# Kernel optimization log

Measured on AMD Instinct MI355X. Metric: run time of the kernel, lower is better.

Reference implementation:

```python
import jax, jax.numpy as jnp
import numpy as np

N, E, EQ = 100000, 600000, 200000
F_IN, HID, N_CONVS = 128, 128, 4  # n_layers=3 -> 4 conv blocks
BN_EPS = 1e-5


def setup_inputs() -> dict:
    key = jax.random.key(0)
    ks = jax.random.split(key, 16)
    s = 1.0 / np.sqrt(HID)
    inp = {
        "x": jax.random.normal(ks[0], (N, F_IN), jnp.float32),
        "edge_index": jax.random.randint(ks[1], (2, E), 0, N, jnp.int64),
        "edge_attr": jax.random.uniform(ks[2], (E,), jnp.float32),
        "edge_label_index": jax.random.randint(ks[3], (2, EQ), 0, N, jnp.int64),
        # GraphConv params (layer 0 has in_dim == hidden_dim, so stack all 4)
        "rel_w": jax.random.normal(ks[4], (N_CONVS, HID, HID), jnp.float32) * s,
        "rel_b": jnp.zeros((N_CONVS, HID), jnp.float32),
        "root_w": jax.random.normal(ks[5], (N_CONVS, HID, HID), jnp.float32) * s,
        "bn_g": jnp.ones((N_CONVS, HID), jnp.float32),
        "bn_b": jnp.zeros((N_CONVS, HID), jnp.float32),
        # edge MLP: Linear(2H->H), GELU, Linear(H->1)
        "mlp_w1": jax.random.normal(ks[6], (2 * HID, HID), jnp.float32) * (1.0 / np.sqrt(2 * HID)),
        "mlp_b1": jnp.zeros((HID,), jnp.float32),
        "mlp_w2": jax.random.normal(ks[7], (HID, 1), jnp.float32) * s,
        "mlp_b2": jnp.zeros((1,), jnp.float32),
    }
    return inp


def reference(x, edge_index, edge_attr, edge_label_index,
              rel_w, rel_b, root_w, bn_g, bn_b,
              mlp_w1, mlp_b1, mlp_w2, mlp_b2):
    src, dst = edge_index[0], edge_index[1]
    n = x.shape[0]
    for l in range(rel_w.shape[0]):
        # GraphConv: lin_rel(sum_j w_ij * x_j) + lin_root(x_i)
        msg = x[src] * edge_attr[:, None]                      # [E, H] gather
        agg = jax.ops.segment_sum(msg, dst, num_segments=n)    # [N, H] scatter-add
        h = agg @ rel_w[l] + rel_b[l] + x @ root_w[l]
        h = jax.nn.gelu(h, approximate=False)
        # BatchNorm over nodes (training-mode batch stats, biased var)
        mean = h.mean(axis=0)
        var = h.var(axis=0)
        x = (h - mean) * jax.lax.rsqrt(var + BN_EPS) * bn_g[l] + bn_b[l]
    ef = jnp.concatenate([x[edge_label_index[0]], x[edge_label_index[1]]], axis=-1)  # [EQ, 2H]
    hmid = jax.nn.gelu(ef @ mlp_w1 + mlp_b1, approximate=False)
    out = jax.nn.sigmoid(hmid @ mlp_w2 + mlp_b2)
    return out.squeeze(-1)
```

## Files before the change

### kernel.cpp

```cpp
#include <hip/hip_runtime.h>

#define NN 100000
#define EE 600000
#define NQ 200000
#define HID 128
#define NL 4
#define BN_EPS 1e-5f
#define ECAP 1280

typedef __attribute__((ext_vector_type(8))) short short8;
typedef __attribute__((ext_vector_type(4))) float f32x4;

__device__ __forceinline__ float gelu_f(float v) {
    return 0.5f * v * (1.0f + erff(v * 0.70710678118654752f));
}
__device__ __forceinline__ unsigned short f2bf(float f) {
    unsigned int x = __float_as_uint(f);
    unsigned int r = (x + 0x7FFFu + ((x >> 16) & 1u)) >> 16;
    return (unsigned short)r;
}
__device__ __forceinline__ float bf2f(unsigned short u) {
    return __uint_as_float(((unsigned int)u) << 16);
}


__global__ void k_zero_int(int* __restrict__ p, int n) {
    int i = blockIdx.x * blockDim.x + threadIdx.x;
    if (i < n) p[i] = 0;
}

__global__ void k_cvt(const float* __restrict__ x, unsigned int* __restrict__ o, int n2) {
    int i = blockIdx.x * blockDim.x + threadIdx.x;
    if (i < n2) {
        float2 v = ((const float2*)x)[i];
        o[i] = (unsigned int)f2bf(v.x) | ((unsigned int)f2bf(v.y) << 16);
    }
}

__global__ void k_bninit(float* __restrict__ sc) {
    int i = threadIdx.x;
    sc[i] = (i < 128) ? 1.0f : 0.0f;
}


__global__ void k_hist(const int* __restrict__ ei, int* __restrict__ cnt) {
    int e = blockIdx.x * blockDim.x + threadIdx.x;
    if (e < EE) atomicAdd(&cnt[ei[EE + e]], 1);
}

__global__ void k_scan1(const int* __restrict__ cnt, int* __restrict__ rp,
                        int* __restrict__ bsum, int n) {
    __shared__ int sh[256];
    const int tid = threadIdx.x;
    const int base = blockIdx.x * 1024;
    int v[4];
    int s = 0;
    #pragma unroll
    for (int j = 0; j < 4; ++j) {
        int idx = base + tid * 4 + j;
        v[j] = (idx < n) ? cnt[idx] : 0;
        s += v[j];
    }
    sh[tid] = s;
    __syncthreads();
    for (int off = 1; off < 256; off <<= 1) {
        int t = (tid >= off) ? sh[tid - off] : 0;
        __syncthreads();
        sh[tid] += t;
        __syncthreads();
    }
    int run = sh[tid] - s;
    #pragma unroll
    for (int j = 0; j < 4; ++j) {
        int idx = base + tid * 4 + j;
        if (idx < n) rp[idx] = run;
        run += v[j];
    }
    if (tid == 255) bsum[blockIdx.x] = sh[255];
}

__global__ void k_scan2(int* __restrict__ bsum, int nb) {
    __shared__ int sh[256];
    const int tid = threadIdx.x;
    int v = (tid < nb) ? bsum[tid] : 0;
    sh[tid] = v;
    __syncthreads();
    for (int off = 1; off < 256; off <<= 1) {
        int t = (tid >= off) ? sh[tid - off] : 0;
        __syncthreads();
        sh[tid] += t;
        __syncthreads();
    }
    if (tid < nb) bsum[tid] = sh[tid] - v;
}

__global__ void k_scan3(int* __restrict__ rp, const int* __restrict__ bsum,
                        int* __restrict__ cnt, int n) {
    int i = blockIdx.x * blockDim.x + threadIdx.x;
    if (i < n) {
        rp[i] += bsum[i >> 10];
        cnt[i] = 0;
    }
    if (i == 0) rp[n] = EE;
}

__global__ void k_fill(const int* __restrict__ ei, const int* __restrict__ rp,
                       int* __restrict__ cur, int* __restrict__ eord) {
    int e = blockIdx.x * blockDim.x + threadIdx.x;
    if (e < EE) {
        int d = ei[EE + e];
        int p = rp[d] + atomicAdd(&cur[d], 1);
        eord[p] = e;
    }
}

__global__ void k_sortfill(const int* __restrict__ ei, const float* __restrict__ ea,
                           const int* __restrict__ rp, int* __restrict__ eord,
                           int* __restrict__ csrc, float* __restrict__ cea,
                           float* __restrict__ wdeg) {
    int n = blockIdx.x * blockDim.x + threadIdx.x;
    if (n >= NN) return;
    const int s0 = rp[n], s1 = rp[n + 1];
    for (int i = s0 + 1; i < s1; ++i) {
        int key = eord[i];
        int j = i - 1;
        while (j >= s0 && eord[j] > key) { eord[j + 1] = eord[j]; --j; }
        eord[j + 1] = key;
    }
    float s = 0.f;
    for (int i = s0; i < s1; ++i) {
        const int e = eord[i];
        csrc[i] = ei[e];
        const float w = ea[e];
        cea[i] = w;
        s += w;
    }
    wdeg[n] = s;
}


__global__ void k_wprep(const float* __restrict__ relw, const float* __restrict__ rootw,
                        const float* __restrict__ relb, const float* __restrict__ sc,
                        unsigned short* __restrict__ Wtf, float* __restrict__ bias2,
                        float* __restrict__ brel) {
    __shared__ float shb[256];
    const int n = blockIdx.x;
    const int k = threadIdx.x;
    const float s = sc[k & 127];
    const float w = (k < 128) ? relw[(size_t)k * HID + n] : rootw[(size_t)(k - 128) * HID + n];
    const int nb = n >> 4, l15 = n & 15;
    const int kc = k >> 5, kg = (k >> 3) & 3, e = k & 7;
    Wtf[((size_t)(kc * 8 + nb) * 512) + (kg * 16 + l15) * 8 + e] = f2bf(s * w);
    shb[k] = sc[128 + (k & 127)] * w;
    __syncthreads();
    #pragma unroll
    for (int off = 64; off >= 1; off >>= 1) {
        if (k < off) shb[k] += shb[k + off];
        else if (k >= 128 && k < 128 + off) shb[k] += shb[k + off];
        __syncthreads();
    }
    if (k == 0) brel[n] = shb[0];
    if (k == 128) bias2[n] = relb[n] + shb[128];
}

__global__ void k_mlpprep(const float* __restrict__ w1, const float* __restrict__ b1,
                          const float* __restrict__ sc, unsigned short* __restrict__ Wtmf,
                          float* __restrict__ b1v) {
    __shared__ float shb[256];
    const int n = blockIdx.x;
    const int k = threadIdx.x;
    const float w = w1[(size_t)k * HID + n];
    const int nb = n >> 4, l15 = n & 15;
    const int kc = k >> 5, kg = (k >> 3) & 3, e = k & 7;
    Wtmf[((size_t)(kc * 8 + nb) * 512) + (kg * 16 + l15) * 8 + e] = f2bf(sc[k & 127] * w);
    shb[k] = sc[128 + (k & 127)] * w;
    __syncthreads();
    #pragma unroll
    for (int off = 128; off >= 1; off >>= 1) {
        if (k < off) shb[k] += shb[k + off];
        __syncthreads();
    }
    if (k == 0) b1v[n] = b1[n] + shb[0];
}


__global__ __launch_bounds__(512, 6) void k_gemm2(
    const unsigned short* __restrict__ hprev, const int* __restrict__ csrc,
    const float* __restrict__ cea, const int* __restrict__ rp,
    const unsigned short* __restrict__ Wtf, const float* __restrict__ bias2,
    const float* __restrict__ brel, const float* __restrict__ wdeg,
    unsigned short* __restrict__ hnext, float* __restrict__ bnpart,
    int nrows, int nblk) {
    __shared__ unsigned short As[128 * 128];
    __shared__ float psb[8 * 64];
    __shared__ float pqb[8 * 64];
    __shared__ int eidx[ECAP];
    __shared__ float ew[ECAP];
    __shared__ int rps[132];
    const int tid = threadIdx.x;
    const int rb = blockIdx.x * 128;

    const int lane = tid & 63;
    const int wid = tid >> 6;
    const int wm = wid >> 1, wn = wid & 1;

    if (tid < 129) {
        int nn = rb + tid;
        rps[tid] = rp[nn < nrows ? nn : nrows];
    }
    __syncthreads();
    const int e0 = rps[0];
    const int ne = rps[128] - e0;
    const bool useLds = (ne <= ECAP);
    if (useLds) {
        for (int i = tid; i < ne; i += 512) {
            eidx[i] = csrc[e0 + i];
            ew[i] = cea[e0 + i];
        }
    }

    f32x4 acc[2][4];
    #pragma unroll
    for (int mf = 0; mf < 2; ++mf)
        #pragma unroll
        for (int nf = 0; nf < 4; ++nf) acc[mf][nf] = (f32x4){0.f, 0.f, 0.f, 0.f};

    #pragma unroll
    for (int s = 0; s < 2; ++s) {
        __syncthreads();
        if (s == 0) {
            const int g = lane >> 4;
            const int cl = lane & 15;
            for (int rr = 0; rr < 16; ++rr) {
                const int r = wid * 16 + rr;
                const int s0 = rps[r] - e0, s1 = rps[r + 1] - e0;
                float a0 = 0.f, a1 = 0.f, a2 = 0.f, a3 = 0.f,
                      a4 = 0.f, a5 = 0.f, a6 = 0.f, a7 = 0.f;
                for (int i = s0 + g; i < s1; i += 8) {
                    const int i2 = i + 4;
                    const bool has2 = i2 < s1;
                    int src1, src2;
                    float w1, w2;
                    if (useLds) {
                        src1 = eidx[i]; w1 = ew[i];
                        src2 = has2 ? eidx[i2] : src1;
                        w2 = has2 ? ew[i2] : 0.f;
                    } else {
                        src1 = csrc[e0 + i]; w1 = cea[e0 + i];
                        src2 = has2 ? csrc[e0 + i2] : src1;
                        w2 = has2 ? cea[e0 + i2] : 0.f;
                    }
                    const uint4 va = *(const uint4*)(hprev + (size_t)src1 * HID + cl * 8);
                    const uint4 vb = *(const uint4*)(hprev + (size_t)src2 * HID + cl * 8);
                    a0 += bf2f((unsigned short)(va.x)) * w1;
                    a1 += bf2f((unsigned short)(va.x >> 16)) * w1;
                    a2 += bf2f((unsigned short)(va.y)) * w1;
                    a3 += bf2f((unsigned short)(va.y >> 16)) * w1;
                    a4 += bf2f((unsigned short)(va.z)) * w1;
                    a5 += bf2f((unsigned short)(va.z >> 16)) * w1;
                    a6 += bf2f((unsigned short)(va.w)) * w1;
                    a7 += bf2f((unsigned short)(va.w >> 16)) * w1;
                    a0 += bf2f((unsigned short)(vb.x)) * w2;
                    a1 += bf2f((unsigned short)(vb.x >> 16)) * w2;
                    a2 += bf2f((unsigned short)(vb.y)) * w2;
                    a3 += bf2f((unsigned short)(vb.y >> 16)) * w2;
                    a4 += bf2f((unsigned short)(vb.z)) * w2;
                    a5 += bf2f((unsigned short)(vb.z >> 16)) * w2;
                    a6 += bf2f((unsigned short)(vb.w)) * w2;
                    a7 += bf2f((unsigned short)(vb.w >> 16)) * w2;
                }
                a0 += __shfl_xor(a0, 16); a1 += __shfl_xor(a1, 16);
                a2 += __shfl_xor(a2, 16); a3 += __shfl_xor(a3, 16);
                a4 += __shfl_xor(a4, 16); a5 += __shfl_xor(a5, 16);
                a6 += __shfl_xor(a6, 16); a7 += __shfl_xor(a7, 16);
                a0 += __shfl_xor(a0, 32); a1 += __shfl_xor(a1, 32);
                a2 += __shfl_xor(a2, 32); a3 += __shfl_xor(a3, 32);
                a4 += __shfl_xor(a4, 32); a5 += __shfl_xor(a5, 32);
                a6 += __shfl_xor(a6, 32); a7 += __shfl_xor(a7, 32);
                if (g == 0) {
                    uint4 o;
                    o.x = (unsigned int)f2bf(a0) | ((unsigned int)f2bf(a1) << 16);
                    o.y = (unsigned int)f2bf(a2) | ((unsigned int)f2bf(a3) << 16);
                    o.z = (unsigned int)f2bf(a4) | ((unsigned int)f2bf(a5) << 16);
                    o.w = (unsigned int)f2bf(a6) | ((unsigned int)f2bf(a7) << 16);
                    const int p = cl ^ (r & 7);
                    *(uint4*)(As + r * 128 + p * 8) = o;
                }
            }
        } else {
            #pragma unroll
            for (int i = 0; i < 4; ++i) {
                const int r = i * 32 + (tid >> 4);
                const int p = tid & 15;
                const int gr = min(rb + r, nrows - 1);
                const int gc = p ^ (r & 7);
                const uint4 v = *(const uint4*)(hprev + (size_t)gr * 128 + gc * 8);
                *(uint4*)(As + r * 128 + p * 8) = v;
            }
        }
        __syncthreads();
        #pragma unroll
        for (int kk = 0; kk < 4; ++kk) {
            short8 a[2], b[4];
            #pragma unroll
            for (int mf = 0; mf < 2; ++mf) {
                const int r = wm * 32 + mf * 16 + (lane & 15);
                const int p = (kk * 4 + (lane >> 4)) ^ (r & 7);
                a[mf] = *(const short8*)(As + r * 128 + p * 8);
            }
            #pragma unroll
            for (int nf = 0; nf < 4; ++nf) {
                b[nf] = *(const short8*)(Wtf + ((size_t)((s * 4 + kk) * 8 + wn * 4 + nf) * 512)
                                               + lane * 8);
            }
            #pragma unroll
            for (int mf = 0; mf < 2; ++mf)
                #pragma unroll
                for (int nf = 0; nf < 4; ++nf)
                    acc[mf][nf] = __builtin_amdgcn_mfma_f32_16x16x32_bf16(
                        a[mf], b[nf], acc[mf][nf], 0, 0, 0);
        }
    }

    __syncthreads();

    int colv[4];
    float biasv[4], brelv[4];
    #pragma unroll
    for (int nf = 0; nf < 4; ++nf) {
        colv[nf] = wn * 64 + nf * 16 + (lane & 15);
        biasv[nf] = bias2[colv[nf]];
        brelv[nf] = brel[colv[nf]];
    }
    float ps[4] = {0.f, 0.f, 0.f, 0.f}, pq[4] = {0.f, 0.f, 0.f, 0.f};
    #pragma unroll
    for (int mf = 0; mf < 2; ++mf) {
        #pragma unroll
        for (int reg = 0; reg < 4; ++reg) {
            const int lr = wm * 32 + mf * 16 + (lane >> 4) * 4 + reg;
            const int gm = rb + lr;
            const bool valid = gm < nrows;
            const float wd = valid ? wdeg[gm] : 0.f;
            #pragma unroll
            for (int nf = 0; nf < 4; ++nf) {
                const float hv = gelu_f(acc[mf][nf][reg] + biasv[nf] + wd * brelv[nf]);
                As[lr * 128 + colv[nf]] = f2bf(hv);
                if (valid) {
                    ps[nf] += hv;
                    pq[nf] += hv * hv;
                }
            }
        }
    }
    #pragma unroll
    for (int nf = 0; nf < 4; ++nf) {
        ps[nf] += __shfl_xor(ps[nf], 16); ps[nf] += __shfl_xor(ps[nf], 32);
        pq[nf] += __shfl_xor(pq[nf], 16); pq[nf] += __shfl_xor(pq[nf], 32);
        if ((lane >> 4) == 0) {
            psb[wid * 64 + nf * 16 + (lane & 15)] = ps[nf];
            pqb[wid * 64 + nf * 16 + (lane & 15)] = pq[nf];
        }
    }
    __syncthreads();

    const int nvalid = nrows - rb;
    #pragma unroll
    for (int it = 0; it < 4; ++it) {
        const int r = it * 32 + (tid >> 4);
        const int c16 = tid & 15;
        if (r < nvalid)
            *(uint4*)(hnext + (size_t)(rb + r) * 128 + c16 * 8) =
                *(const uint4*)(As + r * 128 + c16 * 8);
    }
    if (tid < 128) {
        const int wnh = tid >> 6;
        const int c64 = tid & 63;
        float s = 0.f, q = 0.f;
        #pragma unroll
        for (int w = 0; w < 4; ++w) {
            s += psb[(w * 2 + wnh) * 64 + c64];
            q += pqb[(w * 2 + wnh) * 64 + c64];
        }
        bnpart[(size_t)tid * nblk + blockIdx.x] = s;
        bnpart[(size_t)(128 + tid) * nblk + blockIdx.x] = q;
    }
}

__global__ void k_bnredfin(const float* __restrict__ bnpart, int nblk,
                           const float* __restrict__ g, const float* __restrict__ b,
                           float* __restrict__ sc) {
    __shared__ float sh[256];
    __shared__ float sh2[256];
    const int tid = threadIdx.x;
    const int col = blockIdx.x;
    float s = 0.f, q = 0.f;
    for (int i = tid; i < nblk; i += 256) {
        s += bnpart[(size_t)col * nblk + i];
        q += bnpart[(size_t)(128 + col) * nblk + i];
    }
    sh[tid] = s;
    sh2[tid] = q;
    __syncthreads();
    #pragma unroll
    for (int off = 128; off >= 1; off >>= 1) {
        if (tid < off) { sh[tid] += sh[tid + off]; sh2[tid] += sh2[tid + off]; }
        __syncthreads();
    }
    if (tid == 0) {
        const float inv_n = 1.0f / (float)NN;
        const float mean = sh[0] * inv_n;
        const float var = sh2[0] * inv_n - mean * mean;
        const float scale = g[col] * rsqrtf(var + BN_EPS);
        sc[col] = scale;
        sc[128 + col] = b[col] - mean * scale;
    }
}


__global__ __launch_bounds__(512, 6) void k_mlp2(
    const unsigned short* __restrict__ xf, const int* __restrict__ eli,
    const unsigned short* __restrict__ Wtmf, const float* __restrict__ b1v,
    const float* __restrict__ w2, const float* __restrict__ b2,
    float* __restrict__ out, int nq) {
    __shared__ unsigned short As[128 * 128];
    __shared__ int sidx[256];
    __shared__ float rowred2[2][128];
    const int tid = threadIdx.x;
    const int qb = blockIdx.x * 128;
    if (tid < 256) {
        const int rr = tid & 127;
        const int q = qb + rr;
        sidx[tid] = (q < nq) ? eli[(tid >> 7) * NQ + q] : 0;
    }
    __syncthreads();

    const int lane = tid & 63;
    const int wid = tid >> 6;
    const int wm = wid >> 1, wn = wid & 1;

    f32x4 acc[2][4];
    #pragma unroll
    for (int mf = 0; mf < 2; ++mf)
        #pragma unroll
        for (int nf = 0; nf < 4; ++nf) acc[mf][nf] = (f32x4){0.f, 0.f, 0.f, 0.f};

    #pragma unroll
    for (int s = 0; s < 2; ++s) {
        if (s) __syncthreads();
        #pragma unroll
        for (int i = 0; i < 4; ++i) {
            const int r = i * 32 + (tid >> 4);
            const int p = tid & 15;
            const int node = sidx[s * 128 + r];
            const int gc = p ^ (r & 7);
            const uint4 v = *(const uint4*)(xf + (size_t)node * 128 + gc * 8);
            *(uint4*)(As + r * 128 + p * 8) = v;
        }
        __syncthreads();
        #pragma unroll
        for (int kk = 0; kk < 4; ++kk) {
            short8 a[2], b[4];
            #pragma unroll
            for (int mf = 0; mf < 2; ++mf) {
                const int r = wm * 32 + mf * 16 + (lane & 15);
                const int p = (kk * 4 + (lane >> 4)) ^ (r & 7);
                a[mf] = *(const short8*)(As + r * 128 + p * 8);
            }
            #pragma unroll
            for (int nf = 0; nf < 4; ++nf) {
                b[nf] = *(const short8*)(Wtmf + ((size_t)((s * 4 + kk) * 8 + wn * 4 + nf) * 512)
                                               + lane * 8);
            }
            #pragma unroll
            for (int mf = 0; mf < 2; ++mf)
                #pragma unroll
                for (int nf = 0; nf < 4; ++nf)
                    acc[mf][nf] = __builtin_amdgcn_mfma_f32_16x16x32_bf16(
                        a[mf], b[nf], acc[mf][nf], 0, 0, 0);
        }
    }

    int colv[4];
    float w2v[4], b1c[4];
    #pragma unroll
    for (int nf = 0; nf < 4; ++nf) {
        colv[nf] = wn * 64 + nf * 16 + (lane & 15);
        w2v[nf] = w2[colv[nf]];
        b1c[nf] = b1v[colv[nf]];
    }
    #pragma unroll
    for (int mf = 0; mf < 2; ++mf) {
        #pragma unroll
        for (int reg = 0; reg < 4; ++reg) {
            float part = 0.f;
            #pragma unroll
            for (int nf = 0; nf < 4; ++nf)
                part += gelu_f(acc[mf][nf][reg] + b1c[nf]) * w2v[nf];
            part += __shfl_xor(part, 1);
            part += __shfl_xor(part, 2);
            part += __shfl_xor(part, 4);
            part += __shfl_xor(part, 8);
            if ((lane & 15) == 0) {
                const int lr = wm * 32 + mf * 16 + (lane >> 4) * 4 + reg;
                rowred2[wn][lr] = part;
            }
        }
    }
    __syncthreads();
    if (tid < 128) {
        const int q = qb + tid;
        if (q < nq)
            out[q] = 1.0f / (1.0f + expf(-(rowred2[0][tid] + rowred2[1][tid] + b2[0])));
    }
}


extern "C" void kernel_launch(void* const* d_in, const int* in_sizes, int n_in,
                              void* d_out, int out_size, void* d_ws, size_t ws_size,
                              hipStream_t stream) {
    const float* x_in = (const float*)d_in[0];
    const int* ei = (const int*)d_in[1];
    const float* ea = (const float*)d_in[2];
    const int* eli = (const int*)d_in[3];
    const float* rel_w = (const float*)d_in[4];
    const float* rel_b = (const float*)d_in[5];
    const float* root_w = (const float*)d_in[6];
    const float* bn_g = (const float*)d_in[7];
    const float* bn_b = (const float*)d_in[8];
    const float* w1 = (const float*)d_in[9];
    const float* b1 = (const float*)d_in[10];
    const float* w2 = (const float*)d_in[11];
    const float* b2 = (const float*)d_in[12];
    float* out = (float*)d_out;

    char* ws = (char*)d_ws;
    size_t off = 0;
    auto alloc = [&](size_t bytes) -> void* {
        void* p = ws + off;
        off = (off + bytes + 255) & ~(size_t)255;
        return p;
    };
    const int nblk_gemm = (NN + 127) / 128;
    unsigned short* hb0 = (unsigned short*)alloc(2ull * NN * HID);
    unsigned short* hb1 = (unsigned short*)alloc(2ull * NN * HID);
    int* eord = (int*)alloc(sizeof(int) * EE);
    int* csrc = (int*)alloc(sizeof(int) * EE);
    float* cea = (float*)alloc(sizeof(float) * EE);
    int* rp = (int*)alloc(sizeof(int) * (NN + 1));
    int* cnt = (int*)alloc(sizeof(int) * NN);
    int* bsum = (int*)alloc(sizeof(int) * 256);
    float* wdeg = (float*)alloc(sizeof(float) * NN);
    float* bnpart = (float*)alloc(sizeof(float) * 256 * (size_t)nblk_gemm);
    float* bnsc = (float*)alloc(sizeof(float) * 256);
    unsigned short* Wtf = (unsigned short*)alloc(2ull * 128 * 256);
    unsigned short* Wtmf = (unsigned short*)alloc(2ull * 128 * 256);
    float* bias2 = (float*)alloc(sizeof(float) * 128);
    float* brel = (float*)alloc(sizeof(float) * 128);
    float* b1v = (float*)alloc(sizeof(float) * 128);
    (void)ws_size;

    const int nb_scan = (NN + 1023) / 1024;

    k_cvt<<<(NN * 64 + 255) / 256, 256, 0, stream>>>(x_in, (unsigned int*)hb0, NN * 64);

    k_zero_int<<<(NN + 255) / 256, 256, 0, stream>>>(cnt, NN);
    k_hist<<<(EE + 255) / 256, 256, 0, stream>>>(ei, cnt);
    k_scan1<<<nb_scan, 256, 0, stream>>>(cnt, rp, bsum, NN);
    k_scan2<<<1, 256, 0, stream>>>(bsum, nb_scan);
    k_scan3<<<(NN + 255) / 256, 256, 0, stream>>>(rp, bsum, cnt, NN);
    k_fill<<<(EE + 255) / 256, 256, 0, stream>>>(ei, rp, cnt, eord);
    k_sortfill<<<(NN + 255) / 256, 256, 0, stream>>>(ei, ea, rp, eord, csrc, cea, wdeg);
    k_bninit<<<1, 256, 0, stream>>>(bnsc);

    unsigned short* hcur = hb0;
    unsigned short* bufs[2] = {hb1, hb0};
    for (int l = 0; l < NL; ++l) {
        unsigned short* hnext = bufs[l & 1];
        k_wprep<<<128, 256, 0, stream>>>(rel_w + (size_t)l * HID * HID,
                                         root_w + (size_t)l * HID * HID,
                                         rel_b + (size_t)l * HID, bnsc, Wtf, bias2, brel);
        k_gemm2<<<nblk_gemm, 512, 0, stream>>>(hcur, csrc, cea, rp, Wtf, bias2, brel, wdeg,
                                               hnext, bnpart, NN, nblk_gemm);
        k_bnredfin<<<128, 256, 0, stream>>>(bnpart, nblk_gemm,
                                            bn_g + (size_t)l * HID, bn_b + (size_t)l * HID, bnsc);
        hcur = hnext;
    }

    k_mlpprep<<<128, 256, 0, stream>>>(w1, b1, bnsc, Wtmf, b1v);
    k_mlp2<<<(NQ + 127) / 128, 512, 0, stream>>>(hcur, eli, Wtmf, b1v, w2, b2, out, NQ);
}
```

Baseline: 461.1 us.

## Assign one row per 16-lane group in gather, pack edge data, store output directly

The aggregation phase now gives each 16-lane quarter-wave its own destination row instead of splitting each row's edges across four lane groups. This removes the cross-group shuffle reductions and the lane-0-only write, and uses two independent accumulator sets to keep dependent adds apart. Edge source index and weight are packed into one int2 LDS array so a single LDS load fetches both. The epilogue writes bf16 results straight to global memory as scattered 2-byte stores instead of staging through LDS for coalesced 16-byte writes, which lets one barrier go. The risk is load imbalance between rows of different degree within a wave, and poorer coalescing of the output stores.

```diff
diff --git a/kernel.cpp b/kernel.cpp
--- a/kernel.cpp
+++ b/kernel.cpp
@@ -194,8 +194,7 @@
     __shared__ unsigned short As[128 * 128];
     __shared__ float psb[8 * 64];
     __shared__ float pqb[8 * 64];
-    __shared__ int eidx[ECAP];
-    __shared__ float ew[ECAP];
+    __shared__ int2 ewi[ECAP];
     __shared__ int rps[132];
     const int tid = threadIdx.x;
     const int rb = blockIdx.x * 128;
@@ -214,8 +213,7 @@
     const bool useLds = (ne <= ECAP);
     if (useLds) {
         for (int i = tid; i < ne; i += 512) {
-            eidx[i] = csrc[e0 + i];
-            ew[i] = cea[e0 + i];
+            ewi[i] = make_int2(csrc[e0 + i], __float_as_int(cea[e0 + i]));
         }
     }
 
@@ -231,24 +229,27 @@
         if (s == 0) {
             const int g = lane >> 4;
             const int cl = lane & 15;
-            for (int rr = 0; rr < 16; ++rr) {
-                const int r = wid * 16 + rr;
+            #pragma unroll
+            for (int rs = 0; rs < 4; ++rs) {
+                const int r = wid * 16 + rs * 4 + g;
                 const int s0 = rps[r] - e0, s1 = rps[r + 1] - e0;
                 float a0 = 0.f, a1 = 0.f, a2 = 0.f, a3 = 0.f,
                       a4 = 0.f, a5 = 0.f, a6 = 0.f, a7 = 0.f;
-                for (int i = s0 + g; i < s1; i += 8) {
-                    const int i2 = i + 4;
-                    const bool has2 = i2 < s1;
+                float c0 = 0.f, c1 = 0.f, c2 = 0.f, c3 = 0.f,
+                      c4 = 0.f, c5 = 0.f, c6 = 0.f, c7 = 0.f;
+                for (int i = s0; i < s1; i += 2) {
                     int src1, src2;
                     float w1, w2;
+                    const bool has2 = (i + 1) < s1;
                     if (useLds) {
-                        src1 = eidx[i]; w1 = ew[i];
-                        src2 = has2 ? eidx[i2] : src1;
-                        w2 = has2 ? ew[i2] : 0.f;
+                        const int2 p1 = ewi[i];
+                        src1 = p1.x; w1 = __int_as_float(p1.y);
+                        const int2 p2 = has2 ? ewi[i + 1] : p1;
+                        src2 = p2.x; w2 = has2 ? __int_as_float(p2.y) : 0.f;
                     } else {
                         src1 = csrc[e0 + i]; w1 = cea[e0 + i];
-                        src2 = has2 ? csrc[e0 + i2] : src1;
-                        w2 = has2 ? cea[e0 + i2] : 0.f;
+                        src2 = has2 ? csrc[e0 + i + 1] : src1;
+                        w2 = has2 ? cea[e0 + i + 1] : 0.f;
                     }
                     const uint4 va = *(const uint4*)(hprev + (size_t)src1 * HID + cl * 8);
                     const uint4 vb = *(const uint4*)(hprev + (size_t)src2 * HID + cl * 8);
@@ -260,32 +261,24 @@
                     a5 += bf2f((unsigned short)(va.z >> 16)) * w1;
                     a6 += bf2f((unsigned short)(va.w)) * w1;
                     a7 += bf2f((unsigned short)(va.w >> 16)) * w1;
-                    a0 += bf2f((unsigned short)(vb.x)) * w2;
-                    a1 += bf2f((unsigned short)(vb.x >> 16)) * w2;
-                    a2 += bf2f((unsigned short)(vb.y)) * w2;
-                    a3 += bf2f((unsigned short)(vb.y >> 16)) * w2;
-                    a4 += bf2f((unsigned short)(vb.z)) * w2;
-                    a5 += bf2f((unsigned short)(vb.z >> 16)) * w2;
-                    a6 += bf2f((unsigned short)(vb.w)) * w2;
-                    a7 += bf2f((unsigned short)(vb.w >> 16)) * w2;
+                    c0 += bf2f((unsigned short)(vb.x)) * w2;
+                    c1 += bf2f((unsigned short)(vb.x >> 16)) * w2;
+                    c2 += bf2f((unsigned short)(vb.y)) * w2;
+                    c3 += bf2f((unsigned short)(vb.y >> 16)) * w2;
+                    c4 += bf2f((unsigned short)(vb.z)) * w2;
+                    c5 += bf2f((unsigned short)(vb.z >> 16)) * w2;
+                    c6 += bf2f((unsigned short)(vb.w)) * w2;
+                    c7 += bf2f((unsigned short)(vb.w >> 16)) * w2;
                 }
-                a0 += __shfl_xor(a0, 16); a1 += __shfl_xor(a1, 16);
-                a2 += __shfl_xor(a2, 16); a3 += __shfl_xor(a3, 16);
-                a4 += __shfl_xor(a4, 16); a5 += __shfl_xor(a5, 16);
-                a6 += __shfl_xor(a6, 16); a7 += __shfl_xor(a7, 16);
-                a0 += __shfl_xor(a0, 32); a1 += __shfl_xor(a1, 32);
-                a2 += __shfl_xor(a2, 32); a3 += __shfl_xor(a3, 32);
-                a4 += __shfl_xor(a4, 32); a5 += __shfl_xor(a5, 32);
-                a6 += __shfl_xor(a6, 32); a7 += __shfl_xor(a7, 32);
-                if (g == 0) {
-                    uint4 o;
-                    o.x = (unsigned int)f2bf(a0) | ((unsigned int)f2bf(a1) << 16);
-                    o.y = (unsigned int)f2bf(a2) | ((unsigned int)f2bf(a3) << 16);
-                    o.z = (unsigned int)f2bf(a4) | ((unsigned int)f2bf(a5) << 16);
-                    o.w = (unsigned int)f2bf(a6) | ((unsigned int)f2bf(a7) << 16);
-                    const int p = cl ^ (r & 7);
-                    *(uint4*)(As + r * 128 + p * 8) = o;
-                }
+                a0 += c0; a1 += c1; a2 += c2; a3 += c3;
+                a4 += c4; a5 += c5; a6 += c6; a7 += c7;
+                uint4 o;
+                o.x = (unsigned int)f2bf(a0) | ((unsigned int)f2bf(a1) << 16);
+                o.y = (unsigned int)f2bf(a2) | ((unsigned int)f2bf(a3) << 16);
+                o.z = (unsigned int)f2bf(a4) | ((unsigned int)f2bf(a5) << 16);
+                o.w = (unsigned int)f2bf(a6) | ((unsigned int)f2bf(a7) << 16);
+                const int p = cl ^ (r & 7);
+                *(uint4*)(As + r * 128 + p * 8) = o;
             }
         } else {
             #pragma unroll
@@ -322,8 +315,6 @@
         }
     }
 
-    __syncthreads();
-
     int colv[4];
     float biasv[4], brelv[4];
     #pragma unroll
@@ -337,15 +328,14 @@
     for (int mf = 0; mf < 2; ++mf) {
         #pragma unroll
         for (int reg = 0; reg < 4; ++reg) {
-            const int lr = wm * 32 + mf * 16 + (lane >> 4) * 4 + reg;
-            const int gm = rb + lr;
+            const int gm = rb + wm * 32 + mf * 16 + (lane >> 4) * 4 + reg;
             const bool valid = gm < nrows;
             const float wd = valid ? wdeg[gm] : 0.f;
             #pragma unroll
             for (int nf = 0; nf < 4; ++nf) {
                 const float hv = gelu_f(acc[mf][nf][reg] + biasv[nf] + wd * brelv[nf]);
-                As[lr * 128 + colv[nf]] = f2bf(hv);
                 if (valid) {
+                    hnext[(size_t)gm * 128 + colv[nf]] = f2bf(hv);
                     ps[nf] += hv;
                     pq[nf] += hv * hv;
                 }
@@ -362,16 +352,6 @@
         }
     }
     __syncthreads();
-
-    const int nvalid = nrows - rb;
-    #pragma unroll
-    for (int it = 0; it < 4; ++it) {
-        const int r = it * 32 + (tid >> 4);
-        const int c16 = tid & 15;
-        if (r < nvalid)
-            *(uint4*)(hnext + (size_t)(rb + r) * 128 + c16 * 8) =
-                *(const uint4*)(As + r * 128 + c16 * 8);
-    }
     if (tid < 128) {
         const int wnh = tid >> 6;
         const int c64 = tid & 63;
```

New measurement: 419.2 us. 9.1% less time.
